# Performance work log

Hardware: AMD Instinct MI355X
Metric: run time of the kernel (lower is better)

Reference implementation:

```python
import jax, jax.numpy as jnp
import numpy as np

PLACEHOLDER = -1
B, S, V = 128, 8, 32000  # batch, spec tokens per request, vocab
T = B * S


def setup_inputs() -> dict:
    key = jax.random.key(0)
    ks = jax.random.split(key, 8)
    target_logits = jax.random.normal(ks[0], (T, V), dtype=jnp.float32)
    dp = jax.random.uniform(ks[1], (T, V), dtype=jnp.float32)
    draft_probs = dp / jnp.sum(dp, axis=-1, keepdims=True)  # valid prob dist per token
    draft_token_ids = jax.random.randint(ks[2], (T,), 0, V, dtype=jnp.int32)
    bonus_token_ids = jax.random.randint(ks[3], (B,), 0, V, dtype=jnp.int32)
    temperature = 0.5 + jax.random.uniform(ks[4], (B,), dtype=jnp.float32)  # >0 => all random
    uniform_probs = jax.random.uniform(ks[5], (T,), dtype=jnp.float32)
    # q ~ Exponential(1), as torch's q.exponential_()
    u = jax.random.uniform(ks[6], (B, V), dtype=jnp.float32, minval=1e-10, maxval=1.0)
    q = -jnp.log(u)
    cu_num_draft_tokens = (jnp.arange(B, dtype=jnp.int32) + 1) * S
    return {
        'target_logits': target_logits,
        'draft_probs': draft_probs,
        'draft_token_ids': draft_token_ids,
        'bonus_token_ids': bonus_token_ids,
        'temperature': temperature,
        'uniform_probs': uniform_probs,
        'q': q,
        'cu_num_draft_tokens': cu_num_draft_tokens,
    }


def reference(target_logits, draft_probs, draft_token_ids, bonus_token_ids,
              temperature, uniform_probs, q, cu_num_draft_tokens):
    # compute_probs: softmax of logits / per-token expanded temperature
    temp_tok = jnp.repeat(temperature, S)  # [T]
    target_probs = jax.nn.softmax(target_logits / temp_tok[:, None], axis=-1)  # [T, V]

    tok = jnp.arange(T)
    req = tok // S  # request index per token (uniform raggedness)

    # accept/reject: target_prob/draft_prob >= u  (guard draft_prob > 0)
    p_tgt = target_probs[tok, draft_token_ids]  # [T]
    p_drf = draft_probs[tok, draft_token_ids]   # [T]
    accept = (p_drf > 0) & (p_tgt >= uniform_probs * p_drf)  # [T]

    # recovered tokens: argmax(max(p_tgt - p_drf, 0) / q) over vocab (Gumbel-max trick)
    resid = jnp.maximum(target_probs - draft_probs, 0.0)  # [T, V]
    recovered = jnp.argmax(resid / q[req], axis=-1).astype(jnp.int32)  # [T]

    # sequential accept until first rejection, then placeholder; bonus if all accepted
    accept_b = accept.reshape(B, S)
    alive = jnp.concatenate(
        [jnp.ones((B, 1), dtype=bool),
         jnp.cumprod(accept_b[:, :-1].astype(jnp.int32), axis=1).astype(bool)],
        axis=1)  # alive[b, p] = all accepts before pos p
    tok_out = jnp.where(accept_b, draft_token_ids.reshape(B, S), recovered.reshape(B, S))
    main = jnp.where(alive, tok_out, PLACEHOLDER)  # [B, S]
    all_acc = jnp.all(accept_b, axis=1)
    bonus_col = jnp.where(all_acc, bonus_token_ids, PLACEHOLDER)  # [B]
    output_token_ids = jnp.concatenate([main, bonus_col[:, None]], axis=1)  # [B, S+1]
    return output_token_ids
```

## Files before the change

### kernel.cpp

```cpp
#include <hip/hip_runtime.h>


constexpr int PLACEHOLDER = -1;
constexpr int B = 128;
constexpr int S = 8;
constexpr int V = 32000;
constexpr int T = B * S;
constexpr int NV4 = V / 4;

extern "C" __device__ float __builtin_amdgcn_exp2f(float);
extern "C" __device__ float __builtin_amdgcn_rcpf(float);

__global__ __launch_bounds__(512)
void k1_sum(const float* __restrict__ logits,
            const float* __restrict__ temperature,
            float* __restrict__ w_D)
{
    const int t   = blockIdx.x;
    const int tid = threadIdx.x, lane = tid & 63, wid = tid >> 6;
    __shared__ float s_red[8];

    const float c = 1.4426950408889634f / temperature[t >> 3];
    const float4* lrow = (const float4*)(logits + (size_t)t * V);

    float lsum = 0.f;
    #pragma unroll 4
    for (int j = 0; j < 16; ++j) {
        const int i4 = j * 512 + tid;
        if (i4 < NV4) {
            const float4 v = lrow[i4];
            lsum += (__builtin_amdgcn_exp2f(v.x * c) +
                     __builtin_amdgcn_exp2f(v.y * c)) +
                    (__builtin_amdgcn_exp2f(v.z * c) +
                     __builtin_amdgcn_exp2f(v.w * c));
        }
    }
    #pragma unroll
    for (int off = 32; off >= 1; off >>= 1)
        lsum += __shfl_xor(lsum, off, 64);
    if (lane == 0) s_red[wid] = lsum;
    __syncthreads();
    if (wid == 0) {
        float v = (lane < 8) ? s_red[lane] : 0.f;
        #pragma unroll
        for (int off = 4; off >= 1; off >>= 1)
            v += __shfl_xor(v, off, 64);
        if (lane == 0) w_D[t] = v;
    }
}

__global__ __launch_bounds__(1024, 2)
void k2_fin(const float* __restrict__ logits,
            const float* __restrict__ dprobs,
            const float* __restrict__ q,
            const int*   __restrict__ draft_ids,
            const int*   __restrict__ bonus_ids,
            const float* __restrict__ temperature,
            const float* __restrict__ uniform_probs,
            const float* __restrict__ w_D,
            int* __restrict__ out)
{
    const int b   = blockIdx.x;
    const int tid = threadIdx.x, lane = tid & 63, wid = tid >> 6;
    __shared__ float s_val[16];
    __shared__ int   s_idx[16];
    __shared__ int   s_needp;

    const float c = 1.4426950408889634f / temperature[b];

    if (wid == 0) {
        bool acc = false;
        int  dt  = 0;
        if (lane < S) {
            const int t = b * S + lane;
            dt = draft_ids[t];
            const float l_d = logits[(size_t)t * V + dt];
            const float d_d = dprobs[(size_t)t * V + dt];
            const float u   = uniform_probs[t];
            const float Dv  = w_D[t];
            const float e_d = __builtin_amdgcn_exp2f(l_d * c);
            acc = (d_d > 0.f) && (e_d >= u * d_d * Dv);
        }
        const unsigned long long mask = __ballot(lane < S && acc);
        const unsigned long long rej  = (~mask) & 0xFFull;
        const int need_p = rej ? (int)__builtin_ctzll(rej) : S;
        if (lane < S)
            out[b * (S + 1) + lane] = (lane < need_p) ? dt : PLACEHOLDER;
        if (lane == 0) {
            out[b * (S + 1) + S] = (need_p == S) ? bonus_ids[b] : PLACEHOLDER;
            s_needp = need_p;
        }
    }
    __syncthreads();
    const int need_p = s_needp;
    if (need_p >= S) return;

    const int   t = b * S + need_p;
    const float D = w_D[t];
    const float4* lrow = (const float4*)(logits + (size_t)t * V);
    const float4* drow = (const float4*)(dprobs + (size_t)t * V);
    const float4* qrow = (const float4*)(q      + (size_t)b * V);

    float bestv = -__builtin_inff();
    int   besti = 0x7fffffff;

#define RS_COMP(LC, DC, QC, GIDX)                                          \
    {                                                                      \
        const float e  = __builtin_amdgcn_exp2f((LC) * c);                 \
        const float rq = __builtin_amdgcn_rcpf(QC);                        \
        const float r  = fmaf(-((DC) * rq), D, e * rq);                    \
        if (r > bestv) { bestv = r; besti = (GIDX); }                      \
    }

    #pragma unroll 2
    for (int j = 0; j < 8; ++j) {
        const int i4 = j * 1024 + tid;
        if (i4 < NV4) {
            const float4 lv = lrow[i4];
            const float4 dv = drow[i4];
            const float4 qv = qrow[i4];
            const int base  = i4 * 4;
            RS_COMP(lv.x, dv.x, qv.x, base + 0)
            RS_COMP(lv.y, dv.y, qv.y, base + 1)
            RS_COMP(lv.z, dv.z, qv.z, base + 2)
            RS_COMP(lv.w, dv.w, qv.w, base + 3)
        }
    }
#undef RS_COMP

    #pragma unroll
    for (int off = 32; off >= 1; off >>= 1) {
        const float ov = __shfl_xor(bestv, off, 64);
        const int   oi = __shfl_xor(besti, off, 64);
        if (ov > bestv || (ov == bestv && oi < besti)) { bestv = ov; besti = oi; }
    }
    if (lane == 0) { s_val[wid] = bestv; s_idx[wid] = besti; }
    __syncthreads();
    if (wid == 0) {
        float bv = (lane < 16) ? s_val[lane] : -__builtin_inff();
        int   bi = (lane < 16) ? s_idx[lane] : 0x7fffffff;
        #pragma unroll
        for (int off = 8; off >= 1; off >>= 1) {
            const float ov = __shfl_xor(bv, off, 64);
            const int   oi = __shfl_xor(bi, off, 64);
            if (ov > bv || (ov == bv && oi < bi)) { bv = ov; bi = oi; }
        }
        if (lane == 0)
            out[b * (S + 1) + need_p] = bi;
    }
}

extern "C" void kernel_launch(void* const* d_in, const int* in_sizes, int n_in,
                              void* d_out, int out_size, void* d_ws, size_t ws_size,
                              hipStream_t stream) {
    const float* logits      = (const float*)d_in[0];
    const float* dprobs      = (const float*)d_in[1];
    const int*   draft_ids   = (const int*)d_in[2];
    const int*   bonus_ids   = (const int*)d_in[3];
    const float* temperature = (const float*)d_in[4];
    const float* uniform     = (const float*)d_in[5];
    const float* q           = (const float*)d_in[6];

    int* out = (int*)d_out;
    float* w_D = (float*)d_ws;

    k1_sum<<<T, 512, 0, stream>>>(logits, temperature, w_D);
    k2_fin<<<B, 1024, 0, stream>>>(logits, dprobs, q, draft_ids, bonus_ids,
                                   temperature, uniform, w_D, out);
}
```

Measured before the change: 35.76 us.

## Move accept test into sum kernel and batch loads in residual argmax

The per-token accept/reject test moves into the row-sum kernel, which gathers the draft-token logit, draft prob and uniform at its start and writes an accept flag to workspace. The finish kernel then only reads flags, which shortens its serial prologue before the vocab scan. The residual argmax loop now issues four float4 loads per array before computing, to raise memory-level parallelism. The launch-bounds occupancy hint of 2 is dropped, which frees more registers per thread but may lower occupancy.

```diff
diff --git a/kernel.cpp b/kernel.cpp
--- a/kernel.cpp
+++ b/kernel.cpp
@@ -13,8 +13,12 @@
 
 __global__ __launch_bounds__(512)
 void k1_sum(const float* __restrict__ logits,
+            const float* __restrict__ dprobs,
+            const int*   __restrict__ draft_ids,
             const float* __restrict__ temperature,
-            float* __restrict__ w_D)
+            const float* __restrict__ uniform_probs,
+            float* __restrict__ w_D,
+            int*   __restrict__ w_acc)
 {
     const int t   = blockIdx.x;
     const int tid = threadIdx.x, lane = tid & 63, wid = tid >> 6;
@@ -22,6 +26,14 @@
 
     const float c = 1.4426950408889634f / temperature[t >> 3];
     const float4* lrow = (const float4*)(logits + (size_t)t * V);
+
+    int dt = 0; float l_d = 0.f, d_d = 0.f, u = 0.f;
+    if (tid == 0) {
+        dt  = draft_ids[t];
+        l_d = logits[(size_t)t * V + dt];
+        d_d = dprobs[(size_t)t * V + dt];
+        u   = uniform_probs[t];
+    }
 
     float lsum = 0.f;
     #pragma unroll 4
@@ -40,24 +52,24 @@
         lsum += __shfl_xor(lsum, off, 64);
     if (lane == 0) s_red[wid] = lsum;
     __syncthreads();
-    if (wid == 0) {
-        float v = (lane < 8) ? s_red[lane] : 0.f;
-        #pragma unroll
-        for (int off = 4; off >= 1; off >>= 1)
-            v += __shfl_xor(v, off, 64);
-        if (lane == 0) w_D[t] = v;
+    if (tid == 0) {
+        const float D = ((s_red[0] + s_red[1]) + (s_red[2] + s_red[3])) +
+                        ((s_red[4] + s_red[5]) + (s_red[6] + s_red[7]));
+        w_D[t] = D;
+        const float e_d = __builtin_amdgcn_exp2f(l_d * c);
+        w_acc[t] = (d_d > 0.f) && (e_d >= u * d_d * D);
     }
 }
 
-__global__ __launch_bounds__(1024, 2)
+__global__ __launch_bounds__(1024)
 void k2_fin(const float* __restrict__ logits,
             const float* __restrict__ dprobs,
             const float* __restrict__ q,
             const int*   __restrict__ draft_ids,
             const int*   __restrict__ bonus_ids,
             const float* __restrict__ temperature,
-            const float* __restrict__ uniform_probs,
             const float* __restrict__ w_D,
+            const int*   __restrict__ w_acc,
             int* __restrict__ out)
 {
     const int b   = blockIdx.x;
@@ -69,20 +81,9 @@
     const float c = 1.4426950408889634f / temperature[b];
 
     if (wid == 0) {
-        bool acc = false;
-        int  dt  = 0;
-        if (lane < S) {
-            const int t = b * S + lane;
-            dt = draft_ids[t];
-            const float l_d = logits[(size_t)t * V + dt];
-            const float d_d = dprobs[(size_t)t * V + dt];
-            const float u   = uniform_probs[t];
-            const float Dv  = w_D[t];
-            const float e_d = __builtin_amdgcn_exp2f(l_d * c);
-            acc = (d_d > 0.f) && (e_d >= u * d_d * Dv);
-        }
-        const unsigned long long mask = __ballot(lane < S && acc);
-        const unsigned long long rej  = (~mask) & 0xFFull;
+        const int acc = (lane < S) ? w_acc[b * S + lane] : 1;
+        const int dt  = (lane < S) ? draft_ids[b * S + lane] : 0;
+        const unsigned long long rej = __ballot(lane < S && !acc) & 0xFFull;
         const int need_p = rej ? (int)__builtin_ctzll(rej) : S;
         if (lane < S)
             out[b * (S + 1) + lane] = (lane < need_p) ? dt : PLACEHOLDER;
@@ -112,18 +113,34 @@
         if (r > bestv) { bestv = r; besti = (GIDX); }                      \
     }
 
-    #pragma unroll 2
-    for (int j = 0; j < 8; ++j) {
-        const int i4 = j * 1024 + tid;
-        if (i4 < NV4) {
-            const float4 lv = lrow[i4];
-            const float4 dv = drow[i4];
-            const float4 qv = qrow[i4];
-            const int base  = i4 * 4;
-            RS_COMP(lv.x, dv.x, qv.x, base + 0)
-            RS_COMP(lv.y, dv.y, qv.y, base + 1)
-            RS_COMP(lv.z, dv.z, qv.z, base + 2)
-            RS_COMP(lv.w, dv.w, qv.w, base + 3)
+    #pragma unroll
+    for (int ph = 0; ph < 2; ++ph) {
+        float4 lv[4], dv[4], qv[4];
+        #pragma unroll
+        for (int j = 0; j < 4; ++j) {
+            const int i4 = (ph * 4 + j) * 1024 + tid;
+            if (i4 < NV4) lv[j] = lrow[i4];
+        }
+        #pragma unroll
+        for (int j = 0; j < 4; ++j) {
+            const int i4 = (ph * 4 + j) * 1024 + tid;
+            if (i4 < NV4) dv[j] = drow[i4];
+        }
+        #pragma unroll
+        for (int j = 0; j < 4; ++j) {
+            const int i4 = (ph * 4 + j) * 1024 + tid;
+            if (i4 < NV4) qv[j] = qrow[i4];
+        }
+        #pragma unroll
+        for (int j = 0; j < 4; ++j) {
+            const int i4 = (ph * 4 + j) * 1024 + tid;
+            if (i4 < NV4) {
+                const int base = i4 * 4;
+                RS_COMP(lv[j].x, dv[j].x, qv[j].x, base + 0)
+                RS_COMP(lv[j].y, dv[j].y, qv[j].y, base + 1)
+                RS_COMP(lv[j].z, dv[j].z, qv[j].z, base + 2)
+                RS_COMP(lv[j].w, dv[j].w, qv[j].w, base + 3)
+            }
         }
     }
 #undef RS_COMP
@@ -162,9 +179,11 @@
     const float* q           = (const float*)d_in[6];
 
     int* out = (int*)d_out;
-    float* w_D = (float*)d_ws;
+    float* w_D   = (float*)d_ws;
+    int*   w_acc = (int*)(w_D + T);
 
-    k1_sum<<<T, 512, 0, stream>>>(logits, temperature, w_D);
+    k1_sum<<<T, 512, 0, stream>>>(logits, dprobs, draft_ids, temperature,
+                                  uniform, w_D, w_acc);
     k2_fin<<<B, 1024, 0, stream>>>(logits, dprobs, q, draft_ids, bonus_ids,
-                                   temperature, uniform, w_D, out);
+                                   temperature, w_D, w_acc, out);
 }
```

Result: no change. 36.23 us (+1.3%).
